# Kernel optimization log

Measured on AMD Instinct MI355X. Metric: run time of the kernel, lower is better.

Reference implementation:

```python
import jax, jax.numpy as jnp
import numpy as np

T, B, C = 4, 2, 128
LT, LH, LW = 8, 32, 32
NUM_HEADS = 8
HEAD_DIM = C // NUM_HEADS
THETA = 0.7
V_TH = 1.0
TAU = 2.0  # spikingjelly LIFNode default tau
N_WIN = (2, 2, 2)
TOPK = 4
EPS = 1e-5
ATAN_ALPHA = 2.0  # spikingjelly surrogate.ATan default


@jax.custom_vjp
def spike(x):
    return (x >= 0.0).astype(x.dtype)

def _spike_fwd(x):
    return spike(x), x

def _spike_bwd(x, g):
    s = (jnp.pi / 2.0) * ATAN_ALPHA * x
    return (g * (ATAN_ALPHA / 2.0) / (1.0 + s * s),)

spike.defvjp(_spike_fwd, _spike_bwd)


def lif(x_seq):
    """Multi-step LIF: v'=v+(x-v)/tau, spike at v>=V_TH, hard reset to 0 (detached)."""
    def step(v, x):
        v = v + (x - v) / TAU
        s = spike(v - V_TH)
        v = v * (1.0 - jax.lax.stop_gradient(s))  # detach_reset, v_reset=0
        return v, s
    _, s_seq = jax.lax.scan(step, jnp.zeros_like(x_seq[0]), x_seq)
    return s_seq


def bn(x, gamma, beta):
    # BatchNorm3d(track_running_stats=False) on [T*B, C, D, H, W]: batch stats per channel
    mean = x.mean(axis=(0, 1, 3, 4, 5), keepdims=True)
    var = x.var(axis=(0, 1, 3, 4, 5), keepdims=True)
    shp = (1, 1, -1, 1, 1, 1)
    return (x - mean) * jax.lax.rsqrt(var + EPS) * gamma.reshape(shp) + beta.reshape(shp)


def conv3d(x, w, pad):
    t, b = x.shape[:2]
    y = jax.lax.conv_general_dilated(
        x.reshape((t * b,) + x.shape[2:]), w,
        window_strides=(1, 1, 1), padding=[(pad, pad)] * 3,
        dimension_numbers=('NCDHW', 'OIDHW', 'NCDHW'))
    return y.reshape((t, b) + y.shape[1:])


def cdc_t(x, w):
    out = conv3d(x, w, 1)
    # central-difference temporal term: 1x1x1 conv with summed first/last temporal slices
    kd = w[:, :, 0].sum((-1, -2)) + w[:, :, 2].sum((-1, -2))  # [O, I]
    return out - THETA * jnp.einsum('oi,tbidhw->tbodhw', kd, x)


def to_wins(t):
    wt, wh, ww = N_WIN
    Tn, Bn, Cn, Lt, Lh, Lw = t.shape
    lt, lh, lw = Lt // wt, Lh // wh, Lw // ww
    t = t.reshape(Tn, Bn, Cn, wt, lt, wh, lh, ww, lw)
    t = t.transpose(0, 1, 3, 5, 7, 4, 6, 8, 2)
    return t.reshape(Tn, Bn, wt * wh * ww, lt * lh * lw, Cn)


def setup_inputs() -> dict:
    key = jax.random.key(0)
    ks = jax.random.split(key, 4)
    x = jax.random.normal(ks[0], (T, B, C, LT, LH, LW), jnp.float32)
    qw = jax.random.normal(ks[1], (C, C, 3, 3, 3), jnp.float32) / np.sqrt(C * 27)
    kw = jax.random.normal(ks[2], (C, C), jnp.float32) / np.sqrt(C)
    pw = jax.random.normal(ks[3], (C, C), jnp.float32) / np.sqrt(C)
    ones = jnp.ones((C,), jnp.float32)
    zeros = jnp.zeros((C,), jnp.float32)
    return {"x": x, "qw": qw, "q_gamma": ones, "q_beta": zeros,
            "kw": kw, "k_gamma": ones, "k_beta": zeros,
            "v_gamma": ones, "v_beta": zeros,
            "pw": pw, "p_gamma": ones, "p_beta": zeros}


def reference(x, qw, q_gamma, q_beta, kw, k_gamma, k_beta,
              v_gamma, v_beta, pw, p_gamma, p_beta):
    Tn, Bn, Cn, Lt, Lh, Lw = x.shape
    wt, wh, ww = N_WIN
    num_wins = wt * wh * ww
    lt, lh, lw = Lt // wt, Lh // wh, Lw // ww

    q_real = bn(cdc_t(x, qw), q_gamma, q_beta)
    k_real = bn(jnp.einsum('oi,tbidhw->tbodhw', kw, x), k_gamma, k_beta)

    # region-level routing from pre-spike activations
    q_region = to_wins(q_real).mean(axis=(0, 3))  # [B, W, C]
    k_region = to_wins(k_real).mean(axis=(0, 3))
    a_r = jnp.einsum('bwc,bvc->bwv', q_region, k_region) * (HEAD_DIM ** -0.5)
    k_eff = min(TOPK, num_wins)
    _, idx = jax.lax.top_k(a_r, k_eff)  # [B, W, k]

    q = lif(q_real)
    k = lif(k_real)
    v = lif(bn(x, v_gamma, v_beta))
    q_w = to_wins(q)  # [T,B,W,S,C]
    k_w = to_wins(k)
    v_w = to_wins(v)

    # gather routed windows per (batch, target window), mean-aggregate over top-k
    gather = jax.vmap(lambda src_b, idx_b: src_b[:, idx_b], in_axes=(1, 0), out_axes=1)
    k_agg = gather(k_w, idx).mean(axis=3)  # [T,B,W,S,C]
    v_agg = gather(v_w, idx).mean(axis=3)

    S = q_w.shape[3]
    q_h = q_w.reshape(Tn, Bn, num_wins, S, NUM_HEADS, HEAD_DIM)
    k_h = k_agg.reshape(Tn, Bn, num_wins, S, NUM_HEADS, HEAD_DIM)
    v_h = v_agg.reshape(Tn, Bn, num_wins, S, NUM_HEADS, HEAD_DIM)

    attn = (q_h * k_h).sum(axis=5, keepdims=True)  # [T,B,W,S,H,1]
    attn = lif(attn)
    out = (attn * v_h).reshape(Tn, Bn, num_wins, S, Cn)

    out = out.reshape(Tn, Bn, wt, wh, ww, lt, lh, lw, Cn)
    out = out.transpose(0, 1, 8, 2, 5, 3, 6, 4, 7).reshape(Tn, Bn, Cn, Lt, Lh, Lw)

    out = lif(out)
    out = bn(jnp.einsum('oi,tbidhw->tbodhw', pw, out), p_gamma, p_beta)
    return out
```

## Files before the change

kernel.cpp:

```cpp
#include <hip/hip_runtime.h>

#define TT 4
#define BB 2
#define CC 128
#define DD 8
#define HHH 32
#define WWW 32
#define PP (DD*HHH*WWW)
#define TSTRIDE (BB*CC*PP)
#define NWIN 8
#define SSS 1024
#define NHEAD 8
#define HDIM 16
#define THETA 0.7f
#define VTH 1.0f
#define NPERC (TT*BB*PP)
#define EPSf 1e-5f

typedef unsigned short ushortT;
typedef unsigned char ucharT;
typedef _Float16 half_t;
typedef _Float16 f16x8 __attribute__((ext_vector_type(8)));
typedef float    f32x16 __attribute__((ext_vector_type(16)));

typedef const __attribute__((address_space(1))) void* as1_cvp;
typedef __attribute__((address_space(3))) void* as3_vp;

__global__ __launch_bounds__(256) void prep_wmodT(const float* __restrict__ qw,
                                                  float* __restrict__ wmodT) {
    int oi = blockIdx.x*256 + threadIdx.x;
    if (oi >= CC*CC) return;
    int o  = oi >> 7;
    int ic = oi & 127;
    const float* wp = qw + (size_t)oi*27;
    float kd = 0.f;
    #pragma unroll
    for (int t=0; t<9; t++) kd += wp[t] + wp[18+t];
    #pragma unroll
    for (int t=0; t<27; t++) {
        float v = wp[t] - ((t==13) ? THETA*kd : 0.f);
        wmodT[((size_t)o*27 + t)*CC + ic] = v;
    }
}

__global__ __launch_bounds__(256) void prep_wfrag(const float* __restrict__ wmodT,
                                                  half_t* __restrict__ wfrag) {
    int id = blockIdx.x*256 + threadIdx.x;
    if (id >= 8*27*4*64) return;
    int lane = id & 63;
    int r = id >> 6;
    int m = r & 3; r >>= 2;
    int t = r % 27;
    int kb = r / 27;
    int o   = m*32 + (lane & 31);
    int ic0 = kb*16 + (lane>>5)*8;
    size_t base = ((size_t)(id>>6))*2*64*8 + (size_t)lane*8;
    #pragma unroll
    for (int j=0;j<8;j++){
        float v = wmodT[((size_t)o*27 + t)*CC + ic0 + j];
        half_t h = (half_t)v;
        half_t l = (half_t)(v - (float)h);
        wfrag[base + 0*64*8 + j] = h;
        wfrag[base + 1*64*8 + j] = l;
    }
}

__global__ __launch_bounds__(256) void prep_w1frag2(const float* __restrict__ Wk,
                                                    const float* __restrict__ Wp,
                                                    half_t* __restrict__ fragk,
                                                    half_t* __restrict__ fragp) {
    int id = blockIdx.x*256 + threadIdx.x;
    if (id >= 4096) return;
    const float* W    = (id < 2048) ? Wk : Wp;
    half_t*      frag = (id < 2048) ? fragk : fragp;
    int i2 = id & 2047;
    int lane = i2 & 63;
    int r = i2 >> 6;
    int m = r & 3;
    int kb = r >> 2;
    int o   = m*32 + (lane & 31);
    int ic0 = kb*16 + (lane>>5)*8;
    size_t base = ((size_t)(kb*4+m))*2*64*8 + (size_t)lane*8;
    #pragma unroll
    for (int j=0;j<8;j++){
        float v = W[(size_t)o*CC + ic0 + j];
        half_t h = (half_t)v;
        half_t l = (half_t)(v - (float)h);
        frag[base + 0*64*8 + j] = h;
        frag[base + 1*64*8 + j] = l;
    }
}

__global__ __launch_bounds__(256) void build_xsplit(const float* __restrict__ x,
                                                    half_t* __restrict__ xsp) {
    int id = blockIdx.x*256 + threadIdx.x;
    if (id >= 8*16*8*34*34) return;
    int wt = id % 34; int r = id/34;
    int hp = r % 34;  r /= 34;
    int dz = r % 8;   r /= 8;
    int icg = r & 15; int tb = r >> 4;
    bool inb = (hp>=1) & (hp<=32) & (wt>=1) & (wt<=32);
    half_t h8[8], l8[8];
    #pragma unroll
    for (int j=0;j<8;j++){
        float v = 0.f;
        if (inb)
            v = x[((size_t)(tb*CC + icg*8+j))*PP + (size_t)dz*1024 + (hp-1)*32 + (wt-1)];
        half_t h = (half_t)v;
        half_t l = (half_t)(v - (float)h);
        h8[j]=h; l8[j]=l;
    }
    #pragma unroll
    for (int sp=0; sp<2; sp++){
        size_t gu = (((((size_t)tb*2 + sp)*16 + icg)*8 + dz)*34 + hp)*34 + wt;
        half_t* dst = xsp + gu*8;
        const half_t* src = (sp==0)?h8:l8;
        #pragma unroll
        for (int j=0;j<8;j++) dst[j] = src[j];
    }
}

__global__ __launch_bounds__(512,2) void conv_mfma4(const half_t* __restrict__ xsp,
                                                    const half_t* __restrict__ wfrag,
                                                    float* __restrict__ y) {
    extern __shared__ half_t slab[];
    int tid  = threadIdx.x;
    int wid  = tid >> 6;
    int lane = tid & 63;
    int ln   = lane & 31;
    int half_ = lane >> 5;
    int hg = blockIdx.x;
    int dp = blockIdx.y;
    int tb = blockIdx.z;
    int H0 = hg*4, d0 = dp*2;
    int r  = wid & 3;
    int mh = wid >> 2;

    auto STAGE = [&](int kb, int bsel) {
        half_t* bufp = slab + (size_t)bsel*(3264*8);
        #pragma unroll 1
        for (int k2=0; k2<7; k2++) {
            int u = tid + (k2<<9);
            if (u < 3264) {
                int sp  = (u >= 1632) ? 1 : 0;
                int r1  = u - sp*1632;
                int icg = (r1 >= 816) ? 1 : 0;
                int p2  = r1 - icg*816;
                int dzs = p2/204; int r3 = p2 - dzs*204;
                int hp  = r3/34;  int wt = r3 - hp*34;
                int dd  = d0 - 1 + dzs;
                const half_t* src = ((unsigned)dd < 8u)
                    ? &xsp[((((((size_t)tb*2 + sp)*16 + (kb*2+icg))*8 + dd)*34 + (H0+hp))*34 + wt)*8]
                    : &xsp[(size_t)ln*8];
                __builtin_amdgcn_global_load_lds((as1_cvp)src,
                    (as3_vp)(bufp + (size_t)u*8), 16, 0, 0);
            }
        }
    };

    f32x16 accA[2][2], accB[2][2];
    #pragma unroll
    for (int dt=0;dt<2;dt++)
        #pragma unroll
        for (int mm=0;mm<2;mm++)
            #pragma unroll
            for (int i=0;i<16;i++){ accA[dt][mm][i]=0.f; accB[dt][mm][i]=0.f; }

    f16x8 ca[2][2];
    #pragma unroll
    for (int mm=0;mm<2;mm++)
        #pragma unroll
        for (int sp=0;sp<2;sp++)
            ca[mm][sp] = *(const f16x8*)&wfrag[((((size_t)0*4 + (mh*2+mm))*2+sp)*64 + lane)*8];

    asm volatile("" ::: "memory");
    STAGE(0,0);
    STAGE(1,1);
    asm volatile("" ::: "memory");

    auto KBODY = [&](int kk, f32x16 (&acc)[2][2]) {
        if (kk == 0) {
            if (wid < 3) asm volatile("s_waitcnt vmcnt(7)" ::: "memory");
            else         asm volatile("s_waitcnt vmcnt(6)" ::: "memory");
        } else {
            asm volatile("s_waitcnt vmcnt(63)" ::: "memory");
        }
        __builtin_amdgcn_s_barrier();
        asm volatile("" ::: "memory");
        const half_t* bufp = slab + (size_t)(kk&1)*(3264*8);

        f16x8 cbC[2][2], cbN[2][2];
        #pragma unroll
        for (int dt=0; dt<2; dt++){
            int unitb = dt*204 + r*34 + ln;
            #pragma unroll
            for (int sp=0; sp<2; sp++)
                cbC[dt][sp] = *(const f16x8*)&bufp[(size_t)((sp*2+half_)*816 + unitb)*8];
        }

        #pragma unroll 1
        for (int t=0; t<27; t++) {
            int t2 = (t<26)? t+1 : 26;
            int dz2=t2/9; int rr2=t2-dz2*9; int dh2=rr2/3; int dw2=rr2-dh2*3;
            #pragma unroll
            for (int dt=0; dt<2; dt++){
                int unitb = (dt + dz2)*204 + (r+dh2)*34 + (ln+dw2);
                #pragma unroll
                for (int sp=0; sp<2; sp++)
                    cbN[dt][sp] = *(const f16x8*)&bufp[(size_t)((sp*2+half_)*816 + unitb)*8];
            }
            f16x8 na[2][2];
            int nt  = (t<26)? t+1 : 0;
            int nkb = (t<26)? kk  : ((kk<7)? kk+1 : kk);
            #pragma unroll
            for (int mm=0;mm<2;mm++)
                #pragma unroll
                for (int sp=0;sp<2;sp++)
                    na[mm][sp] = *(const f16x8*)&wfrag[((((size_t)(nkb*27+nt)*4+(mh*2+mm))*2+sp)*64 + lane)*8];
            #pragma unroll
            for (int dt=0;dt<2;dt++)
                #pragma unroll
                for (int mm=0;mm<2;mm++) acc[dt][mm] = __builtin_amdgcn_mfma_f32_32x32x16_f16(ca[mm][0], cbC[dt][0], acc[dt][mm],0,0,0);
            #pragma unroll
            for (int dt=0;dt<2;dt++)
                #pragma unroll
                for (int mm=0;mm<2;mm++) acc[dt][mm] = __builtin_amdgcn_mfma_f32_32x32x16_f16(ca[mm][0], cbC[dt][1], acc[dt][mm],0,0,0);
            #pragma unroll
            for (int dt=0;dt<2;dt++)
                #pragma unroll
                for (int mm=0;mm<2;mm++) acc[dt][mm] = __builtin_amdgcn_mfma_f32_32x32x16_f16(ca[mm][1], cbC[dt][0], acc[dt][mm],0,0,0);
            #pragma unroll
            for (int dt=0;dt<2;dt++)
                #pragma unroll
                for (int sp=0;sp<2;sp++) cbC[dt][sp] = cbN[dt][sp];
            #pragma unroll
            for (int mm=0;mm<2;mm++)
                #pragma unroll
                for (int sp=0;sp<2;sp++) ca[mm][sp] = na[mm][sp];
        }
        asm volatile("" ::: "memory");
        __builtin_amdgcn_s_barrier();
        asm volatile("" ::: "memory");
        if (kk < 6) STAGE(kk+2, kk&1);
    };

    #pragma unroll 1
    for (int kk=0; kk<4; kk++) KBODY(kk, accA);
    #pragma unroll 1
    for (int kk=4; kk<8; kk++) KBODY(kk, accB);

    int h = H0 + r;
    #pragma unroll
    for (int dt=0; dt<2; dt++) {
        int d = d0 + dt;
        #pragma unroll
        for (int mm=0; mm<2; mm++) {
            #pragma unroll
            for (int reg=0; reg<16; reg++) {
                int row = (reg&3) + 8*(reg>>2) + 4*half_;
                int o = (mh*2+mm)*32 + row;
                y[((size_t)tb*CC + o)*PP + d*1024 + h*32 + ln]
                    = accA[dt][mm][reg] + accB[dt][mm][reg];
            }
        }
    }
}

__global__ __launch_bounds__(256) void kgemm_mfma(const half_t* __restrict__ xsp,
                                                  const half_t* __restrict__ wk,
                                                  float* __restrict__ y) {
    int tid  = threadIdx.x;
    int wid  = tid >> 6;
    int lane = tid & 63;
    int ln   = lane & 31;
    int half_ = lane >> 5;
    int hg = blockIdx.x, d = blockIdx.y, tb = blockIdx.z;
    int h = hg*4 + wid;

    f32x16 acc[4];
    #pragma unroll
    for (int m=0;m<4;m++)
        #pragma unroll
        for (int i=0;i<16;i++) acc[m][i] = 0.f;

    #pragma unroll 2
    for (int kb=0; kb<8; kb++) {
        f16x8 b[2];
        #pragma unroll
        for (int sp=0; sp<2; sp++) {
            size_t gu = (((((size_t)tb*2 + sp)*16 + (kb*2+half_))*8 + d)*34 + (h+1))*34 + (ln+1);
            b[sp] = *(const f16x8*)&xsp[gu*8];
        }
        #pragma unroll
        for (int m=0; m<4; m++) {
            const half_t* wb = wk + ((size_t)(kb*4+m))*2*64*8 + (size_t)lane*8;
            f16x8 a0 = *(const f16x8*)&wb[0*64*8];
            f16x8 a1 = *(const f16x8*)&wb[1*64*8];
            acc[m] = __builtin_amdgcn_mfma_f32_32x32x16_f16(a0, b[0], acc[m],0,0,0);
            acc[m] = __builtin_amdgcn_mfma_f32_32x32x16_f16(a0, b[1], acc[m],0,0,0);
            acc[m] = __builtin_amdgcn_mfma_f32_32x32x16_f16(a1, b[0], acc[m],0,0,0);
        }
    }
    #pragma unroll
    for (int m=0; m<4; m++) {
        #pragma unroll
        for (int reg=0; reg<16; reg++) {
            int row = (reg&3) + 8*(reg>>2) + 4*half_;
            int o = m*32 + row;
            y[((size_t)tb*CC + o)*PP + d*1024 + h*32 + ln] = acc[m][reg];
        }
    }
}

__global__ __launch_bounds__(256) void pgemm_mfma(const ushortT* __restrict__ spkb,
                                                  const half_t* __restrict__ wp,
                                                  float* __restrict__ y) {
    int tid  = threadIdx.x;
    int wid  = tid >> 6;
    int lane = tid & 63;
    int ln   = lane & 31;
    int half_ = lane >> 5;
    int hg = blockIdx.x, d = blockIdx.y, tb = blockIdx.z;
    int h = hg*4 + wid;
    int p = d*1024 + h*32 + ln;

    f32x16 acc[4];
    #pragma unroll
    for (int m=0;m<4;m++)
        #pragma unroll
        for (int i=0;i<16;i++) acc[m][i] = 0.f;

    #pragma unroll 2
    for (int kb=0; kb<8; kb++) {
        f16x8 b = *(const f16x8*)&spkb[(((size_t)tb*16 + (kb*2+half_))*PP + p)*8];
        #pragma unroll
        for (int m=0; m<4; m++) {
            const half_t* wb = wp + ((size_t)(kb*4+m))*2*64*8 + (size_t)lane*8;
            f16x8 a0 = *(const f16x8*)&wb[0*64*8];
            f16x8 a1 = *(const f16x8*)&wb[1*64*8];
            acc[m] = __builtin_amdgcn_mfma_f32_32x32x16_f16(a0, b, acc[m],0,0,0);
            acc[m] = __builtin_amdgcn_mfma_f32_32x32x16_f16(a1, b, acc[m],0,0,0);
        }
    }
    #pragma unroll
    for (int m=0; m<4; m++) {
        #pragma unroll
        for (int reg=0; reg<16; reg++) {
            int row = (reg&3) + 8*(reg>>2) + 4*half_;
            int o = m*32 + row;
            y[((size_t)tb*CC + o)*PP + p] = acc[m][reg];
        }
    }
}

__global__ __launch_bounds__(128) void win_stats(const float* __restrict__ q,
        const float* __restrict__ k, const float* __restrict__ x,
        float* __restrict__ rsum, float* __restrict__ rsq) {
    int blk = blockIdx.x;
    int src = blk >> 11;
    int r   = blk & 2047;
    const float* base = (src==0) ? q : ((src==1) ? k : x);
    int c  = r & 127;
    int wi = (r >> 7) & 7;
    int b  = r >> 10;
    int wd = wi>>2, wh = (wi>>1)&1, ww = wi&1;
    int tid = threadIdx.x;
    float s=0.f, s2=0.f;
    for (int t=0;t<TT;t++){
        const float* p = base + ((size_t)(t*BB+b)*CC + c)*PP;
        for (int si=tid; si<SSS; si+=128){
            int ld = si>>8, lh=(si>>4)&15, lw=si&15;
            float v = p[((wd*4+ld)<<10) + ((wh*16+lh)<<5) + (ww*16+lw)];
            s += v; s2 += v*v;
        }
    }
    __shared__ float ls[128], ls2[128];
    ls[tid]=s; ls2[tid]=s2; __syncthreads();
    for (int off=64;off>0;off>>=1){
        if(tid<off){ ls[tid]+=ls[tid+off]; ls2[tid]+=ls2[tid+off]; }
        __syncthreads();
    }
    if (tid==0){ rsum[blk]=ls[0]; rsq[blk]=ls2[0]; }
}

__global__ __launch_bounds__(384) void route_fin(const float* __restrict__ rsum,
        const float* __restrict__ rsq,
        const float* __restrict__ qg, const float* __restrict__ qb,
        const float* __restrict__ kg, const float* __restrict__ kb,
        float* __restrict__ stats, int* __restrict__ idxout) {
    __shared__ float qn[16*128], kn[16*128], ar[16*8];
    __shared__ float csum[384], csq[384];
    int tid = threadIdx.x;
    {
        int src = tid >> 7, c = tid & 127;
        float s=0.f, s2=0.f;
        for (int bw=0; bw<16; bw++){
            int idx = src*2048 + bw*128 + c;
            s  += rsum[idx];
            s2 += rsq[idx];
        }
        stats[src*256 + c]       = s;
        stats[src*256 + 128 + c] = s2;
        csum[tid]=s; csq[tid]=s2;
    }
    __syncthreads();
    for (int e=tid; e<16*128; e+=384){
        int c = e&127;
        float qm = csum[c]*(1.f/NPERC);
        float qv = csq[c]*(1.f/NPERC) - qm*qm;
        float qr = rsqrtf(qv + EPSf);
        qn[e] = (rsum[e]*(1.f/(TT*SSS)) - qm)*qr*qg[c] + qb[c];
        float km = csum[128+c]*(1.f/NPERC);
        float kv = csq[128+c]*(1.f/NPERC) - km*km;
        float kr = rsqrtf(kv + EPSf);
        kn[e] = (rsum[2048+e]*(1.f/(TT*SSS)) - km)*kr*kg[c] + kb[c];
    }
    __syncthreads();
    if (tid < 128){
        int b = tid>>6, w=(tid>>3)&7, v=tid&7;
        float s=0.f;
        for (int c=0;c<128;c++) s += qn[(b*8+w)*128+c]*kn[(b*8+v)*128+c];
        ar[(b*8+w)*8+v] = s * 0.25f;
    }
    __syncthreads();
    if (tid < 16){
        const float* row = &ar[tid*8];
        bool used[8] = {false,false,false,false,false,false,false,false};
        for (int j=0;j<4;j++){
            int best=0; float bv=-3.0e38f;
            for (int v=0; v<8; v++){
                if (!used[v] && row[v] > bv){ bv=row[v]; best=v; }
            }
            used[best]=true;
            idxout[tid*4+j]=best;
        }
    }
}

__global__ __launch_bounds__(256) void lif_bn_win3(const float* __restrict__ qin,
        const float* __restrict__ kin, const float* __restrict__ xin,
        ucharT* __restrict__ qs, ucharT* __restrict__ ks, ucharT* __restrict__ vs,
        const float* __restrict__ stats,
        const float* __restrict__ qg, const float* __restrict__ qb,
        const float* __restrict__ kg, const float* __restrict__ kb,
        const float* __restrict__ vg, const float* __restrict__ vb) {
    int src = blockIdx.y;
    const float* in  = (src==0) ? qin : ((src==1) ? kin : xin);
    ucharT*      spk = (src==0) ? qs  : ((src==1) ? ks  : vs);
    const float* gamma = (src==0) ? qg : ((src==1) ? kg : vg);
    const float* beta  = (src==0) ? qb : ((src==1) ? kb : vb);
    int e = blockIdx.x*256 + threadIdx.x;
    if (e >= BB*CC*PP) return;
    int p = e & (PP-1);
    int c = (e >> 13) & 127;
    int b = e >> 20;
    float mean = stats[src*256 + c]*(1.f/NPERC);
    float var  = stats[src*256 + 128 + c]*(1.f/NPERC) - mean*mean;
    float sc = rsqrtf(var+EPSf)*gamma[c];
    float sh = beta[c] - mean*sc;
    int d = p>>10, h=(p>>5)&31, w=p&31;
    int wi = ((d>>2)*2 + (h>>4))*2 + (w>>4);
    int si = (((d&3)<<4) + (h&15))*16 + (w&15);
    size_t widx = ((size_t)(b*NWIN+wi)*CC + c)*SSS + si;
    float v=0.f;
    #pragma unroll
    for (int t=0;t<TT;t++){
        float xn = in[(size_t)t*TSTRIDE + e]*sc + sh;
        v = (v+xn)*0.5f;
        float s = (v>=VTH)?1.f:0.f;
        spk[(size_t)t*TSTRIDE + widx] = (ucharT)(v>=VTH ? 1 : 0);
        v *= (1.f - s);
    }
}

__global__ __launch_bounds__(256) void attn_lif(const ucharT* __restrict__ qspk,
        const ucharT* __restrict__ kspk, const ucharT* __restrict__ vspk,
        const int* __restrict__ idx, ushortT* __restrict__ spkb) {
    int id = blockIdx.x*256 + threadIdx.x;
    if (id >= BB*NWIN*NHEAD*SSS) return;
    int s  = id & 1023;
    int hh = (id>>10) & 7;
    int wi = (id>>13) & 7;
    int b  = id>>16;
    int bw = b*NWIN+wi;
    size_t qbase = ((size_t)bw*CC + hh*HDIM)*SSS + s;
    size_t sbase[4];
    #pragma unroll
    for (int j=0;j<4;j++){
        int src = idx[bw*4+j];
        sbase[j] = ((size_t)(b*NWIN+src)*CC + hh*HDIM)*SSS + s;
    }
    int wd = wi>>2, wh = (wi>>1)&1, ww = wi&1;
    int d3 = wd*4 + (s>>8), h3 = wh*16 + ((s>>4)&15), w3 = ww*16 + (s&15);
    int p  = (d3<<10) + (h3<<5) + w3;

    float v=0.f;
    float v2[16];
    #pragma unroll
    for (int dd=0; dd<16; dd++) v2[dd]=0.f;

    #pragma unroll 1
    for (int t=0;t<TT;t++){
        size_t toff = (size_t)t*TSTRIDE;
        int km[16], vm[16];
        #pragma unroll
        for (int dd=0;dd<16;dd++){ km[dd]=0; vm[dd]=0; }
        #pragma unroll
        for (int j=0;j<4;j++){
            const ucharT* kp = kspk+toff+sbase[j];
            const ucharT* vp = vspk+toff+sbase[j];
            #pragma unroll
            for (int dd=0; dd<16; dd++){
                km[dd] += kp[(size_t)dd*SSS];
                vm[dd] += vp[(size_t)dd*SSS];
            }
        }
        const ucharT* qp = qspk+toff+qbase;
        int atti=0;
        #pragma unroll
        for (int dd=0;dd<16;dd++) atti += (int)qp[(size_t)dd*SSS]*km[dd];
        float att = (float)atti * 0.25f;
        v = (v+att)*0.5f;
        float sp = (v>=VTH)?1.f:0.f;
        v *= (1.f-sp);
        float spq = sp*0.25f;
        union { ushortT u[8]; uint4 q4; } pk0, pk1;
        #pragma unroll
        for (int dd=0;dd<16;dd++){
            float ov = spq*(float)vm[dd];
            v2[dd] = (v2[dd]+ov)*0.5f;
            float s2 = (v2[dd]>=VTH)?1.f:0.f;
            v2[dd] *= (1.f-s2);
            ushortT bs = (s2 != 0.f) ? (ushortT)0x3C00 : (ushortT)0;
            if (dd < 8) pk0.u[dd] = bs; else pk1.u[dd-8] = bs;
        }
        int tb2 = t*BB + b;
        size_t base = (((size_t)tb2*16 + hh*2)*PP + p)*8;
        *(uint4*)&spkb[base] = pk0.q4;
        *(uint4*)&spkb[base + (size_t)PP*8] = pk1.q4;
    }
}

__global__ __launch_bounds__(256) void pstats_part(const float* __restrict__ xin,
        float* __restrict__ part_sum, float* __restrict__ part_sq) {
    int blk = blockIdx.x;
    int c = blk & 127, tb = blk >> 7;
    int tid = threadIdx.x;
    const float* p = xin + ((size_t)tb*CC + c)*PP;
    float s=0.f, s2=0.f;
    for (int i=tid; i<PP; i+=256){ float v=p[i]; s+=v; s2+=v*v; }
    __shared__ float ls[256], ls2[256];
    ls[tid]=s; ls2[tid]=s2; __syncthreads();
    for (int off=128; off>0; off>>=1){
        if (tid<off){ ls[tid]+=ls[tid+off]; ls2[tid]+=ls2[tid+off]; }
        __syncthreads();
    }
    if (tid==0){ part_sum[blk]=ls[0]; part_sq[blk]=ls2[0]; }
}

__global__ __launch_bounds__(256) void bn_apply(const float* __restrict__ xin,
        float* __restrict__ yout,
        const float* __restrict__ part_sum, const float* __restrict__ part_sq,
        const float* __restrict__ gamma, const float* __restrict__ beta) {
    size_t i = (size_t)blockIdx.x*256 + threadIdx.x;
    if (i >= (size_t)TT*BB*CC*PP) return;
    int c = (int)((i>>13)&127);
    float s=0.f, s2=0.f;
    #pragma unroll
    for (int tb=0; tb<8; tb++){
        s  += part_sum[tb*128+c];
        s2 += part_sq[tb*128+c];
    }
    float mean = s*(1.f/NPERC);
    float var  = s2*(1.f/NPERC) - mean*mean;
    float sc = rsqrtf(var+EPSf)*gamma[c];
    float sh = beta[c] - mean*sc;
    yout[i] = xin[i]*sc + sh;
}

extern "C" void kernel_launch(void* const* d_in, const int* in_sizes, int n_in,
                              void* d_out, int out_size, void* d_ws, size_t ws_size,
                              hipStream_t stream) {
    const float* x  = (const float*)d_in[0];
    const float* qw = (const float*)d_in[1];
    const float* qg = (const float*)d_in[2];
    const float* qb = (const float*)d_in[3];
    const float* kw = (const float*)d_in[4];
    const float* kg = (const float*)d_in[5];
    const float* kb = (const float*)d_in[6];
    const float* vg = (const float*)d_in[7];
    const float* vb = (const float*)d_in[8];
    const float* pw = (const float*)d_in[9];
    const float* pg = (const float*)d_in[10];
    const float* pb = (const float*)d_in[11];
    float* out = (float*)d_out;
    float* ws  = (float*)d_ws;

    const size_t NEL = (size_t)TT*TSTRIDE;
    float* qconv = ws;
    half_t* xsp  = (half_t*)(ws + 2*NEL);
    const size_t KCONV_OFF = 2*NEL + 10747904;
    float* kconv = ws + KCONV_OFF;
    float* wf_base = ws + KCONV_OFF + NEL;
    half_t* wfrag  = (half_t*)wf_base;
    half_t* wkfrag = (half_t*)(wf_base + 442368);
    float*  wmodT  = wf_base + 442368 + 16384;
    half_t* wpfrag = (half_t*)(wf_base + 442368 + 16384 + 442368);
    float* stats = ws + 5*NEL;
    float* rsum = stats + 1024;
    float* rsq  = rsum + 6144;
    float* ppart_sum = rsq + 6144;
    float* ppart_sq  = ppart_sum + 1024;
    int*   idxp = (int*)(ppart_sq + 1024);

    ucharT* qspk = (ucharT*)(ws + 2*NEL);
    ucharT* kspk = (ucharT*)(ws + 2*NEL) + 8388608;
    ucharT* vspk = (ucharT*)(ws + 2*NEL) + 16777216;
    ushortT* spkb  = (ushortT*)ws;
    float*  pconv  = ws + KCONV_OFF;

    prep_wmodT<<<64,256,0,stream>>>(qw, wmodT);
    prep_wfrag<<<216,256,0,stream>>>(wmodT, wfrag);
    prep_w1frag2<<<16,256,0,stream>>>(kw, pw, wkfrag, wpfrag);
    build_xsplit<<<4624,256,0,stream>>>(x, xsp);
    {
        static bool attr_set = false;
        const int shmem = 2*3264*8*(int)sizeof(half_t);
        if (!attr_set) {
            hipFuncSetAttribute((const void*)conv_mfma4,
                                hipFuncAttributeMaxDynamicSharedMemorySize, shmem);
            attr_set = true;
        }
        dim3 cg(8,4,8);
        conv_mfma4<<<cg,512,shmem,stream>>>(xsp, wfrag, qconv);
    }
    {
        dim3 gg(8,8,8);
        kgemm_mfma<<<gg,256,0,stream>>>(xsp, wkfrag, kconv);
    }
    win_stats<<<6144,128,0,stream>>>(qconv, kconv, x, rsum, rsq);
    route_fin<<<1,384,0,stream>>>(rsum, rsq, qg,qb,kg,kb, stats, idxp);
    {
        dim3 lg(8192,3);
        lif_bn_win3<<<lg,256,0,stream>>>(qconv,kconv,x,
                                         qspk,kspk,vspk,
                                         stats, qg,qb,kg,kb,vg,vb);
    }
    attn_lif<<<512,256,0,stream>>>(qspk,kspk,vspk,idxp,spkb);
    {
        dim3 gg(8,8,8);
        pgemm_mfma<<<gg,256,0,stream>>>(spkb, wpfrag, pconv);
    }
    pstats_part<<<1024,256,0,stream>>>(pconv, ppart_sum, ppart_sq);
    bn_apply<<<32768,256,0,stream>>>(pconv, out, ppart_sum, ppart_sq, pg, pb);
}
```

Before: 390.4 us.

## Vectorize LIF/attention spike kernels with packed byte SIMD and fuse weight prep

lif_bn_win3 now has each thread process four consecutive positions, using float4 loads and one packed 32-bit spike store, so the grid is a quarter the size. attn_lif is reorganized so each thread handles four spatial positions by four head dims. It uses 32-bit packed-byte loads, SWAR masking for the q·k dot product, and lane shuffles to reduce across head-dim groups. The separate prep_wmodT kernel and its intermediate buffer are folded into prep_wfrag, removing one launch at the cost of some redundant weight reads. The packed-byte sums rely on each per-byte count staying within 8 bits.

```diff
diff --git a/kernel.cpp b/kernel.cpp
--- a/kernel.cpp
+++ b/kernel.cpp
@@ -19,6 +19,7 @@
 
 typedef unsigned short ushortT;
 typedef unsigned char ucharT;
+typedef unsigned int uintT;
 typedef _Float16 half_t;
 typedef _Float16 f16x8 __attribute__((ext_vector_type(8)));
 typedef float    f32x16 __attribute__((ext_vector_type(16)));
@@ -26,24 +27,7 @@
 typedef const __attribute__((address_space(1))) void* as1_cvp;
 typedef __attribute__((address_space(3))) void* as3_vp;
 
-__global__ __launch_bounds__(256) void prep_wmodT(const float* __restrict__ qw,
-                                                  float* __restrict__ wmodT) {
-    int oi = blockIdx.x*256 + threadIdx.x;
-    if (oi >= CC*CC) return;
-    int o  = oi >> 7;
-    int ic = oi & 127;
-    const float* wp = qw + (size_t)oi*27;
-    float kd = 0.f;
-    #pragma unroll
-    for (int t=0; t<9; t++) kd += wp[t] + wp[18+t];
-    #pragma unroll
-    for (int t=0; t<27; t++) {
-        float v = wp[t] - ((t==13) ? THETA*kd : 0.f);
-        wmodT[((size_t)o*27 + t)*CC + ic] = v;
-    }
-}
-
-__global__ __launch_bounds__(256) void prep_wfrag(const float* __restrict__ wmodT,
+__global__ __launch_bounds__(256) void prep_wfrag(const float* __restrict__ qw,
                                                   half_t* __restrict__ wfrag) {
     int id = blockIdx.x*256 + threadIdx.x;
     if (id >= 8*27*4*64) return;
@@ -57,7 +41,14 @@
     size_t base = ((size_t)(id>>6))*2*64*8 + (size_t)lane*8;
     #pragma unroll
     for (int j=0;j<8;j++){
-        float v = wmodT[((size_t)o*27 + t)*CC + ic0 + j];
+        const float* wp = qw + ((size_t)o*CC + ic0 + j)*27;
+        float v = wp[t];
+        if (t == 13) {
+            float kd = 0.f;
+            #pragma unroll
+            for (int tt=0; tt<9; tt++) kd += wp[tt] + wp[18+tt];
+            v -= THETA*kd;
+        }
         half_t h = (half_t)v;
         half_t l = (half_t)(v - (float)h);
         wfrag[base + 0*64*8 + j] = h;
@@ -449,8 +440,9 @@
     ucharT*      spk = (src==0) ? qs  : ((src==1) ? ks  : vs);
     const float* gamma = (src==0) ? qg : ((src==1) ? kg : vg);
     const float* beta  = (src==0) ? qb : ((src==1) ? kb : vb);
-    int e = blockIdx.x*256 + threadIdx.x;
-    if (e >= BB*CC*PP) return;
+    int e4 = blockIdx.x*256 + threadIdx.x;
+    if (e4 >= BB*CC*PP/4) return;
+    int e = e4*4;
     int p = e & (PP-1);
     int c = (e >> 13) & 127;
     int b = e >> 20;
@@ -462,14 +454,21 @@
     int wi = ((d>>2)*2 + (h>>4))*2 + (w>>4);
     int si = (((d&3)<<4) + (h&15))*16 + (w&15);
     size_t widx = ((size_t)(b*NWIN+wi)*CC + c)*SSS + si;
-    float v=0.f;
+    float v[4] = {0.f,0.f,0.f,0.f};
     #pragma unroll
     for (int t=0;t<TT;t++){
-        float xn = in[(size_t)t*TSTRIDE + e]*sc + sh;
-        v = (v+xn)*0.5f;
-        float s = (v>=VTH)?1.f:0.f;
-        spk[(size_t)t*TSTRIDE + widx] = (ucharT)(v>=VTH ? 1 : 0);
-        v *= (1.f - s);
+        float4 raw = *(const float4*)&in[(size_t)t*TSTRIDE + e];
+        float xs[4] = {raw.x, raw.y, raw.z, raw.w};
+        uintT pack = 0;
+        #pragma unroll
+        for (int i=0;i<4;i++){
+            float xn = xs[i]*sc + sh;
+            v[i] = (v[i]+xn)*0.5f;
+            float s = (v[i]>=VTH)?1.f:0.f;
+            pack |= (v[i]>=VTH ? 1u : 0u) << (8*i);
+            v[i] *= (1.f - s);
+        }
+        *(uintT*)&spk[(size_t)t*TSTRIDE + widx] = pack;
     }
 }
 
@@ -477,67 +476,81 @@
         const ucharT* __restrict__ kspk, const ucharT* __restrict__ vspk,
         const int* __restrict__ idx, ushortT* __restrict__ spkb) {
     int id = blockIdx.x*256 + threadIdx.x;
-    if (id >= BB*NWIN*NHEAD*SSS) return;
-    int s  = id & 1023;
-    int hh = (id>>10) & 7;
-    int wi = (id>>13) & 7;
-    int b  = id>>16;
-    int bw = b*NWIN+wi;
-    size_t qbase = ((size_t)bw*CC + hh*HDIM)*SSS + s;
+    int ddq = id & 3;
+    int s4  = (id>>2) & 255;
+    int hh  = (id>>10) & 7;
+    int wi  = (id>>13) & 7;
+    int b   = id>>16;
+    int bw  = b*NWIN+wi;
+    int s0  = s4*4;
+    int dd0 = ddq*4;
+    size_t qbase = ((size_t)bw*CC + hh*HDIM + dd0)*SSS + s0;
     size_t sbase[4];
     #pragma unroll
     for (int j=0;j<4;j++){
-        int src = idx[bw*4+j];
-        sbase[j] = ((size_t)(b*NWIN+src)*CC + hh*HDIM)*SSS + s;
+        int srcw = idx[bw*4+j];
+        sbase[j] = ((size_t)(b*NWIN+srcw)*CC + hh*HDIM + dd0)*SSS + s0;
     }
     int wd = wi>>2, wh = (wi>>1)&1, ww = wi&1;
-    int d3 = wd*4 + (s>>8), h3 = wh*16 + ((s>>4)&15), w3 = ww*16 + (s&15);
-    int p  = (d3<<10) + (h3<<5) + w3;
-
-    float v=0.f;
-    float v2[16];
-    #pragma unroll
-    for (int dd=0; dd<16; dd++) v2[dd]=0.f;
+    int d3 = wd*4 + (s0>>8), h3 = wh*16 + ((s0>>4)&15), w3 = ww*16 + (s0&15);
+    int p0 = (d3<<10) + (h3<<5) + w3;
+    int icg  = hh*2 + (ddq>>1);
+    int slot = (ddq&1)*4;
+
+    float v[4] = {0.f,0.f,0.f,0.f};
+    float v2[4][4];
+    #pragma unroll
+    for (int i=0;i<4;i++)
+        #pragma unroll
+        for (int si=0;si<4;si++) v2[i][si]=0.f;
 
     #pragma unroll 1
     for (int t=0;t<TT;t++){
         size_t toff = (size_t)t*TSTRIDE;
-        int km[16], vm[16];
-        #pragma unroll
-        for (int dd=0;dd<16;dd++){ km[dd]=0; vm[dd]=0; }
+        uintT km[4] = {0,0,0,0}, vm[4] = {0,0,0,0};
         #pragma unroll
         for (int j=0;j<4;j++){
             const ucharT* kp = kspk+toff+sbase[j];
             const ucharT* vp = vspk+toff+sbase[j];
             #pragma unroll
-            for (int dd=0; dd<16; dd++){
-                km[dd] += kp[(size_t)dd*SSS];
-                vm[dd] += vp[(size_t)dd*SSS];
+            for (int i=0; i<4; i++){
+                km[i] += *(const uintT*)&kp[(size_t)i*SSS];
+                vm[i] += *(const uintT*)&vp[(size_t)i*SSS];
             }
         }
         const ucharT* qp = qspk+toff+qbase;
-        int atti=0;
-        #pragma unroll
-        for (int dd=0;dd<16;dd++) atti += (int)qp[(size_t)dd*SSS]*km[dd];
-        float att = (float)atti * 0.25f;
-        v = (v+att)*0.5f;
-        float sp = (v>=VTH)?1.f:0.f;
-        v *= (1.f-sp);
-        float spq = sp*0.25f;
-        union { ushortT u[8]; uint4 q4; } pk0, pk1;
-        #pragma unroll
-        for (int dd=0;dd<16;dd++){
-            float ov = spq*(float)vm[dd];
-            v2[dd] = (v2[dd]+ov)*0.5f;
-            float s2 = (v2[dd]>=VTH)?1.f:0.f;
-            v2[dd] *= (1.f-s2);
-            ushortT bs = (s2 != 0.f) ? (ushortT)0x3C00 : (ushortT)0;
-            if (dd < 8) pk0.u[dd] = bs; else pk1.u[dd-8] = bs;
-        }
+        uintT atti = 0;
+        #pragma unroll
+        for (int i=0;i<4;i++){
+            uintT q4 = *(const uintT*)&qp[(size_t)i*SSS];
+            uintT tq = (q4 + 0x7F7F7F7Fu) & 0x80808080u;
+            uintT mask = tq - (tq >> 7);
+            atti += km[i] & mask;
+        }
+        atti += (uintT)__shfl_xor((int)atti, 1);
+        atti += (uintT)__shfl_xor((int)atti, 2);
         int tb2 = t*BB + b;
-        size_t base = (((size_t)tb2*16 + hh*2)*PP + p)*8;
-        *(uint4*)&spkb[base] = pk0.q4;
-        *(uint4*)&spkb[base + (size_t)PP*8] = pk1.q4;
+        size_t obase = (((size_t)tb2*16 + icg)*PP + p0)*8 + slot;
+        #pragma unroll
+        for (int si=0; si<4; si++){
+            float att = (float)((atti >> (8*si)) & 255u) * 0.25f;
+            v[si] = (v[si]+att)*0.5f;
+            float sp = (v[si]>=VTH)?1.f:0.f;
+            v[si] *= (1.f-sp);
+            float spq = sp*0.25f;
+            uintT lo=0, hi=0;
+            #pragma unroll
+            for (int i=0;i<4;i++){
+                float ov = spq*(float)((vm[i] >> (8*si)) & 255u);
+                v2[i][si] = (v2[i][si]+ov)*0.5f;
+                float s2 = (v2[i][si]>=VTH)?1.f:0.f;
+                v2[i][si] *= (1.f-s2);
+                uintT bs = (s2 != 0.f) ? 0x3C00u : 0u;
+                if (i<2) lo |= bs << (16*i); else hi |= bs << (16*(i-2));
+            }
+            uint2 pk; pk.x = lo; pk.y = hi;
+            *(uint2*)&spkb[obase + (size_t)si*8] = pk;
+        }
     }
 }
 
@@ -604,7 +617,6 @@
     float* wf_base = ws + KCONV_OFF + NEL;
     half_t* wfrag  = (half_t*)wf_base;
     half_t* wkfrag = (half_t*)(wf_base + 442368);
-    float*  wmodT  = wf_base + 442368 + 16384;
     half_t* wpfrag = (half_t*)(wf_base + 442368 + 16384 + 442368);
     float* stats = ws + 5*NEL;
     float* rsum = stats + 1024;
@@ -619,8 +631,7 @@
     ushortT* spkb  = (ushortT*)ws;
     float*  pconv  = ws + KCONV_OFF;
 
-    prep_wmodT<<<64,256,0,stream>>>(qw, wmodT);
-    prep_wfrag<<<216,256,0,stream>>>(wmodT, wfrag);
+    prep_wfrag<<<216,256,0,stream>>>(qw, wfrag);
     prep_w1frag2<<<16,256,0,stream>>>(kw, pw, wkfrag, wpfrag);
     build_xsplit<<<4624,256,0,stream>>>(x, xsp);
     {
@@ -641,7 +652,7 @@
     win_stats<<<6144,128,0,stream>>>(qconv, kconv, x, rsum, rsq);
     route_fin<<<1,384,0,stream>>>(rsum, rsq, qg,qb,kg,kb, stats, idxp);
     {
-        dim3 lg(8192,3);
+        dim3 lg(2048,3);
         lif_bn_win3<<<lg,256,0,stream>>>(qconv,kconv,x,
                                          qspk,kspk,vspk,
                                          stats, qg,qb,kg,kb,vg,vb);
```

Measured after the change: 385.8 us. Within noise of the previous version (-1.2%).
